# Kernel tuning notes

Measured on AMD Instinct MI355X. Metric: run time of the kernel, lower is better.

The kernel has to match this reference:

```python
import jax, jax.numpy as jnp
import numpy as np

N = 50000      # nodes
E = 800000     # edges
F_IN = 512     # num_features
H = 128        # hidden


def setup_inputs() -> dict:
    key = jax.random.key(0)
    ks = jax.random.split(key, 10)
    edge_index = jax.random.randint(ks[0], (2, E), 0, N, dtype=jnp.int64 if jax.config.jax_enable_x64 else jnp.int32)
    x = jax.random.normal(ks[1], (N, F_IN), jnp.float32)
    weights = jax.random.uniform(ks[2], (E,), jnp.float32)
    def w(i, shape, fan):
        return jax.random.normal(ks[i], shape, jnp.float32) / np.sqrt(fan).astype(np.float32)
    return {
        "edge_index": edge_index,
        "x": x,
        "weights": weights,
        "W_lin1": w(3, (F_IN, H), F_IN), "b_lin1": jnp.zeros((H,), jnp.float32),
        "W_conv1": w(4, (H, 2 * H), H), "b_conv1": jnp.zeros((2 * H,), jnp.float32),
        "W_mu": w(5, (2 * H, H), 2 * H), "b_mu": jnp.zeros((H,), jnp.float32),
        "W_lin": w(6, (2 * H, 1), 2 * H), "b_lin": jnp.zeros((1,), jnp.float32),
    }


def gcn_conv(x, W, b, src, dst, ew, n):
    """PyG GCNConv with edge weights: add self-loops (weight 1), symmetric norm, scatter-add."""
    loop = jnp.arange(n, dtype=src.dtype)
    s2 = jnp.concatenate([src, loop])
    d2 = jnp.concatenate([dst, loop])
    w2 = jnp.concatenate([ew, jnp.ones((n,), x.dtype)])
    deg = jax.ops.segment_sum(w2, d2, num_segments=n)          # weighted in-degree incl. self-loop
    dinv = jnp.where(deg > 0, deg, 1.0) ** -0.5
    dinv = jnp.where(deg > 0, dinv, 0.0)
    norm = dinv[s2] * w2 * dinv[d2]                            # [E+N]
    h = x @ W                                                   # [N, out]
    out = jax.ops.segment_sum(h[s2] * norm[:, None], d2, num_segments=n)
    return out + b


def reference(edge_index, x, weights, W_lin1, b_lin1, W_conv1, b_conv1, W_mu, b_mu, W_lin, b_lin):
    n = x.shape[0]
    src, dst = edge_index[0], edge_index[1]
    # eval mode: dropout is identity, VGAE.encode returns mu
    h = x @ W_lin1 + b_lin1                                     # lin1
    h = jax.nn.relu(gcn_conv(h, W_conv1, b_conv1, src, dst, weights, n))
    z = gcn_conv(h, W_mu, b_mu, src, dst, weights, n)           # mu == embeddings
    emb_edges = jnp.concatenate([z[src], z[dst]], axis=1)       # [E, 2H]
    out = jax.nn.sigmoid(emb_edges @ W_lin + b_lin)
    return out.squeeze(-1)                                      # [E]
```

## Files before the change

### kernel.cpp

```cpp
#include <hip/hip_runtime.h>
#include <hip/hip_bf16.h>
#include <math.h>


#define NSL 256
#define RSH 8
#define RNG 256

typedef __attribute__((ext_vector_type(8))) short bf16x8;
typedef __attribute__((ext_vector_type(4))) float f32x4;

static __device__ __forceinline__ ushort f2b(float f) {
    __hip_bfloat16 h = __float2bfloat16(f);
    return *(ushort*)&h;
}
static __device__ __forceinline__ float b2f(ushort u) {
    unsigned int v = ((unsigned int)u) << 16;
    return *(float*)&v;
}
static __device__ __forceinline__ bf16x8 cvt8(float4 a, float4 b) {
    bf16x8 r;
    r[0] = (short)f2b(a.x); r[1] = (short)f2b(a.y); r[2] = (short)f2b(a.z); r[3] = (short)f2b(a.w);
    r[4] = (short)f2b(b.x); r[5] = (short)f2b(b.y); r[6] = (short)f2b(b.z); r[7] = (short)f2b(b.w);
    return r;
}


__global__ __launch_bounds__(256) void bucket_count(const int* __restrict__ dst,
                                                    int* __restrict__ cntA, int E, int NR) {
    __shared__ int lc[256];
    const int b = blockIdx.x, t = threadIdx.x;
    lc[t] = 0;
    __syncthreads();
    const int beg = (int)((long long)b * E / NSL);
    const int end = (int)((long long)(b + 1) * E / NSL);
    for (int e = beg + t; e < end; e += 256) atomicAdd(&lc[dst[e] >> RSH], 1);
    __syncthreads();
    if (t < NR) cntA[b * NR + t] = lc[t];
}

__global__ __launch_bounds__(256) void range_scan(int* __restrict__ cntA,
                                                  int* __restrict__ rtot, int NR) {
    __shared__ int s_[256];
    const int r = blockIdx.x, t = threadIdx.x;
    int v = cntA[t * NR + r];
    s_[t] = v;
    __syncthreads();
    for (int off = 1; off < 256; off <<= 1) {
        int add = (t >= off) ? s_[t - off] : 0;
        __syncthreads();
        s_[t] += add;
        __syncthreads();
    }
    cntA[t * NR + r] = s_[t] - v;
    if (t == 255) rtot[r] = s_[t];
}

__global__ __launch_bounds__(256) void base_scan(const int* __restrict__ rtot,
                                                 int* __restrict__ baseOut, int NR) {
    __shared__ int s_[256];
    const int t = threadIdx.x;
    int v = (t < NR) ? rtot[t] : 0;
    s_[t] = v;
    __syncthreads();
    for (int off = 1; off < 256; off <<= 1) {
        int add = (t >= off) ? s_[t - off] : 0;
        __syncthreads();
        s_[t] += add;
        __syncthreads();
    }
    if (t < NR) baseOut[t] = s_[t] - v;
    if (t == NR - 1) baseOut[NR] = s_[t];
}

__global__ __launch_bounds__(256) void bucket_scatter(const int* __restrict__ src,
                                                      const int* __restrict__ dst,
                                                      const float* __restrict__ w,
                                                      const int* __restrict__ cntA,
                                                      const int* __restrict__ baseOut,
                                                      unsigned int* __restrict__ packB,
                                                      float* __restrict__ wB, int E, int NR) {
    __shared__ int cur[256];
    const int b = blockIdx.x, t = threadIdx.x;
    if (t < NR) cur[t] = cntA[b * NR + t] + baseOut[t];
    __syncthreads();
    const int beg = (int)((long long)b * E / NSL);
    const int end = (int)((long long)(b + 1) * E / NSL);
    for (int e = beg + t; e < end; e += 256) {
        int d = dst[e];
        int r = d >> RSH;
        int pos = atomicAdd(&cur[r], 1);
        packB[pos] = ((unsigned int)(d & (RNG - 1)) << 24) | (unsigned int)src[e];
        wB[pos] = w[e];
    }
}

__global__ __launch_bounds__(256) void range_deg(const unsigned int* __restrict__ packB,
                                                 const float* __restrict__ wB,
                                                 const int* __restrict__ baseOut,
                                                 float* __restrict__ dinv,
                                                 int* __restrict__ offs,
                                                 int N, int E) {
    __shared__ float lw[256];
    __shared__ int lc[256];
    __shared__ int sc[256];
    const int r = blockIdx.x, t = threadIdx.x;
    lw[t] = 0.f; lc[t] = 0;
    __syncthreads();
    const int beg = baseOut[r], end = baseOut[r + 1];
    for (int e = beg + t; e < end; e += 256) {
        unsigned int pk = packB[e];
        int dl = pk >> 24;
        atomicAdd(&lc[dl], 1);
        atomicAdd(&lw[dl], wB[e]);
    }
    __syncthreads();
    int v = lc[t];
    sc[t] = v;
    __syncthreads();
    for (int off = 1; off < 256; off <<= 1) {
        int add = (t >= off) ? sc[t - off] : 0;
        __syncthreads();
        sc[t] += add;
        __syncthreads();
    }
    int node = (r << RSH) + t;
    if (node < N) {
        dinv[node] = 1.0f / sqrtf(1.0f + lw[t]);
        offs[node] = beg + sc[t] - v;
    }
    if (r == 0 && t == 0) offs[N] = E;
}

__global__ __launch_bounds__(256) void csr_build(const unsigned int* __restrict__ packB,
                                                 const float* __restrict__ wB,
                                                 const int* __restrict__ baseOut,
                                                 const float* __restrict__ dinv,
                                                 const int* __restrict__ offs,
                                                 int* __restrict__ es,
                                                 float* __restrict__ en, int N) {
    __shared__ int cur[256];
    __shared__ float ldv[256];
    const int r = blockIdx.x, t = threadIdx.x;
    const int node = (r << RSH) + t;
    cur[t] = (node < N) ? offs[node] : 0;
    ldv[t] = (node < N) ? dinv[node] : 0.f;
    __syncthreads();
    const int beg = baseOut[r], end = baseOut[r + 1];
    for (int e = beg + t; e < end; e += 256) {
        unsigned int pk = packB[e];
        int dl = pk >> 24;
        int s = pk & 0xFFFFFF;
        float nrm = dinv[s] * wB[e] * ldv[dl];
        int pos = atomicAdd(&cur[dl], 1);
        es[pos] = s;
        en[pos] = nrm;
    }
}


__global__ __launch_bounds__(256) void tconv_kernel(const float* __restrict__ B,
                                                    ushort* __restrict__ BT, int K, int Nn) {
    int i = blockIdx.x * 256 + threadIdx.x;
    if (i < K * Nn) {
        int k = i / Nn, n = i % Nn;
        BT[(size_t)n * K + k] = f2b(B[i]);
    }
}

__global__ __launch_bounds__(256) void fold_kernel(const float* __restrict__ Wm,
                                                   const float* __restrict__ Wl,
                                                   const float* __restrict__ bm,
                                                   float* __restrict__ wmp,
                                                   float* __restrict__ wmq,
                                                   float* __restrict__ bpq) {
    int j = threadIdx.x;
    float sp = 0.f, sq = 0.f;
    for (int k = 0; k < 128; ++k) {
        float v = Wm[(size_t)j * 128 + k];
        sp += v * Wl[k];
        sq += v * Wl[128 + k];
    }
    wmp[j] = sp; wmq[j] = sq;
    if (j == 0) { float s = 0.f; for (int k = 0; k < 128; ++k) s += bm[k] * Wl[k];       bpq[0] = s; }
    if (j == 1) { float s = 0.f; for (int k = 0; k < 128; ++k) s += bm[k] * Wl[128 + k]; bpq[1] = s; }
}

__global__ __launch_bounds__(64) void gemm1_stream(const float* __restrict__ A,
                                                   const ushort* __restrict__ BT,
                                                   const float* __restrict__ bias,
                                                   ushort* __restrict__ C, int M) {
    const int lane = threadIdx.x;
    const int r0 = blockIdx.x * 16;
    const int lrow = lane & 15;
    const int lk   = (lane >> 4) * 8;

    f32x4 acc[8] = {};

    const float*  a  = A  + (size_t)min(r0 + lrow, M - 1) * 512 + lk;
    const ushort* bp = BT + (size_t)lrow * 512 + lk;

#pragma unroll 4
    for (int ks = 0; ks < 16; ++ks) {
        const int k0 = ks * 32;
        float4 aa = *(const float4*)(a + k0);
        float4 ab = *(const float4*)(a + k0 + 4);
        bf16x8 af = cvt8(aa, ab);
#pragma unroll
        for (int ni = 0; ni < 8; ++ni) {
            bf16x8 bfr = *(const bf16x8*)(bp + (size_t)ni * 16 * 512 + k0);
            acc[ni] = __builtin_amdgcn_mfma_f32_16x16x32_bf16(af, bfr, acc[ni], 0, 0, 0);
        }
    }

#pragma unroll
    for (int ni = 0; ni < 8; ++ni) {
        int col = ni * 16 + lrow;
        float bv = bias[col];
#pragma unroll
        for (int r = 0; r < 4; ++r) {
            int row = r0 + (lane >> 4) * 4 + r;
            if (row < M) C[(size_t)row * 128 + col] = f2b(acc[ni][r] + bv);
        }
    }
}

__global__ __launch_bounds__(256) void aggregate_bf16(const ushort* __restrict__ h,
                                                      const int* __restrict__ offs,
                                                      const int* __restrict__ es,
                                                      const float* __restrict__ en,
                                                      const float* __restrict__ dinv,
                                                      ushort* __restrict__ out, int n) {
    int wave = (int)((blockIdx.x * (size_t)blockDim.x + threadIdx.x) >> 6);
    int lane = threadIdx.x & 63;
    if (wave >= n) return;
    float di = dinv[wave];
    float sw = di * di;
    unsigned int hv = *(const unsigned int*)(h + (size_t)wave * 128 + lane * 2);
    float ax = sw * b2f((ushort)(hv & 0xffff));
    float ay = sw * b2f((ushort)(hv >> 16));
    int beg = offs[wave], end = offs[wave + 1];
    for (int e = beg; e < end; e += 8) {
        int sx[8]; float wx[8];
#pragma unroll
        for (int j = 0; j < 8; ++j) {
            bool v = (e + j) < end;
            sx[j] = v ? es[e + j] : wave;
            wx[j] = v ? en[e + j] : 0.f;
        }
        unsigned int vv[8];
#pragma unroll
        for (int j = 0; j < 8; ++j)
            vv[j] = *(const unsigned int*)(h + (size_t)sx[j] * 128 + lane * 2);
#pragma unroll
        for (int j = 0; j < 8; ++j) {
            ax += wx[j] * b2f((ushort)(vv[j] & 0xffff));
            ay += wx[j] * b2f((ushort)(vv[j] >> 16));
        }
    }
    unsigned int o = (unsigned int)f2b(ax) | ((unsigned int)f2b(ay) << 16);
    *(unsigned int*)(out + (size_t)wave * 128 + lane * 2) = o;
}

__global__ __launch_bounds__(64) void gemm2_stream(const ushort* __restrict__ A,
                                                   const ushort* __restrict__ BT,
                                                   const float* __restrict__ bc,
                                                   const float* __restrict__ wmp,
                                                   const float* __restrict__ wmq,
                                                   float* __restrict__ pe,
                                                   float* __restrict__ qe, int M) {
    const int lane = threadIdx.x;
    const int r0 = blockIdx.x * 16;
    const int lrow = lane & 15;
    const int lk   = (lane >> 4) * 8;

    f32x4 acc[16] = {};

    const ushort* a  = A  + (size_t)min(r0 + lrow, M - 1) * 128 + lk;
    const ushort* bp = BT + (size_t)lrow * 128 + lk;

#pragma unroll
    for (int ks = 0; ks < 4; ++ks) {
        const int k0 = ks * 32;
        bf16x8 af = *(const bf16x8*)(a + k0);
#pragma unroll
        for (int ni = 0; ni < 16; ++ni) {
            bf16x8 bfr = *(const bf16x8*)(bp + (size_t)ni * 16 * 128 + k0);
            acc[ni] = __builtin_amdgcn_mfma_f32_16x16x32_bf16(af, bfr, acc[ni], 0, 0, 0);
        }
    }

    float bcv[16], wpv[16], wqv[16];
#pragma unroll
    for (int ni = 0; ni < 16; ++ni) {
        int col = ni * 16 + lrow;
        bcv[ni] = bc[col];
        wpv[ni] = wmp[col];
        wqv[ni] = wmq[col];
    }
#pragma unroll
    for (int r = 0; r < 4; ++r) {
        float sp = 0.f, sq = 0.f;
#pragma unroll
        for (int ni = 0; ni < 16; ++ni) {
            float h = fmaxf(acc[ni][r] + bcv[ni], 0.f);
            sp += h * wpv[ni];
            sq += h * wqv[ni];
        }
#pragma unroll
        for (int off = 1; off < 16; off <<= 1) {
            sp += __shfl_xor(sp, off);
            sq += __shfl_xor(sq, off);
        }
        if (lrow == 0) {
            int row = r0 + (lane >> 4) * 4 + r;
            if (row < M) { pe[row] = sp; qe[row] = sq; }
        }
    }
}

__global__ __launch_bounds__(256) void agg_scalar(const float* __restrict__ pe,
                                                  const float* __restrict__ qe,
                                                  const int* __restrict__ offs,
                                                  const int* __restrict__ es,
                                                  const float* __restrict__ en,
                                                  const float* __restrict__ dinv,
                                                  const float* __restrict__ bpq,
                                                  float* __restrict__ p,
                                                  float* __restrict__ q, int n) {
    int i = blockIdx.x * 256 + threadIdx.x;
    if (i >= n) return;
    float di = dinv[i];
    float sw = di * di;
    float ap = sw * pe[i], aq = sw * qe[i];
    int beg = offs[i], end = offs[i + 1];
    for (int k = beg; k < end; k += 4) {
        int sx[4]; float wx[4];
#pragma unroll
        for (int j = 0; j < 4; ++j) {
            bool v = (k + j) < end;
            sx[j] = v ? es[k + j] : i;
            wx[j] = v ? en[k + j] : 0.f;
        }
        float pv[4], qv[4];
#pragma unroll
        for (int j = 0; j < 4; ++j) { pv[j] = pe[sx[j]]; qv[j] = qe[sx[j]]; }
#pragma unroll
        for (int j = 0; j < 4; ++j) { ap += wx[j] * pv[j]; aq += wx[j] * qv[j]; }
    }
    p[i] = ap + bpq[0];
    q[i] = aq + bpq[1];
}

__global__ __launch_bounds__(256) void edge_out_kernel(const int* __restrict__ src,
                                                       const int* __restrict__ dst,
                                                       const float* __restrict__ p,
                                                       const float* __restrict__ q,
                                                       const float* __restrict__ bl,
                                                       float* __restrict__ out, int e) {
    int i = blockIdx.x * 256 + threadIdx.x;
    if (i < e) {
        float t = p[src[i]] + q[dst[i]] + bl[0];
        out[i] = 1.0f / (1.0f + expf(-t));
    }
}


extern "C" void kernel_launch(void* const* d_in, const int* in_sizes, int n_in,
                              void* d_out, int out_size, void* d_ws, size_t ws_size,
                              hipStream_t stream) {
    const int*   edge_index = (const int*)d_in[0];
    const float* x   = (const float*)d_in[1];
    const float* w   = (const float*)d_in[2];
    const float* W1  = (const float*)d_in[3];
    const float* b1  = (const float*)d_in[4];
    const float* Wc  = (const float*)d_in[5];
    const float* bc  = (const float*)d_in[6];
    const float* Wm  = (const float*)d_in[7];
    const float* bm  = (const float*)d_in[8];
    const float* Wl  = (const float*)d_in[9];
    const float* bl  = (const float*)d_in[10];
    float* out = (float*)d_out;

    const int E  = in_sizes[2];
    const int H  = in_sizes[4];
    const int F  = in_sizes[3] / H;
    const int N  = in_sizes[1] / F;
    const int H2 = 2 * H;
    const int NR = (N + RNG - 1) / RNG;

    const int* src = edge_index;
    const int* dst = edge_index + E;

    char* ws = (char*)d_ws;
    size_t off = 0;
    auto alloc = [&](size_t bytes) -> void* {
        off = (off + 255) & ~(size_t)255;
        void* r = ws + off;
        off += bytes;
        return r;
    };
    int*          cntA    = (int*)         alloc((size_t)NSL * NR * 4);
    int*          rtot    = (int*)         alloc((size_t)NR * 4);
    int*          baseOut = (int*)         alloc((size_t)(NR + 1) * 4);
    unsigned int* packB   = (unsigned int*)alloc((size_t)E * 4);
    float*        wB      = (float*)       alloc((size_t)E * 4);
    float*        dinv    = (float*)       alloc((size_t)N * 4);
    int*          offs    = (int*)         alloc((size_t)(N + 1) * 4);
    int*          es      = (int*)         alloc((size_t)E * 4);
    float*        en      = (float*)       alloc((size_t)E * 4);
    ushort*       h0_bf   = (ushort*)      alloc((size_t)N * H * 2);
    ushort*       agg1_bf = (ushort*)      alloc((size_t)N * H * 2);
    ushort*       W1T     = (ushort*)      alloc((size_t)H * F * 2);
    ushort*       WcT     = (ushort*)      alloc((size_t)H2 * H * 2);
    float*        wmp     = (float*)       alloc(H2 * 4);
    float*        wmq     = (float*)       alloc(H2 * 4);
    float*        bpq     = (float*)       alloc(2 * 4);
    float*        pe      = (float*)       alloc((size_t)N * 4);
    float*        qe      = (float*)       alloc((size_t)N * 4);
    float*        p       = (float*)       alloc((size_t)N * 4);
    float*        q       = (float*)       alloc((size_t)N * 4);
    (void)ws_size; (void)n_in; (void)out_size;

    int nbN  = (N + 255) / 256;
    int nbE  = (E + 255) / 256;
    int nbW  = (int)(((size_t)N * 64 + 255) / 256);
    int nb16 = (N + 15) / 16;

    bucket_count<<<NSL, 256, 0, stream>>>(dst, cntA, E, NR);
    range_scan<<<NR, 256, 0, stream>>>(cntA, rtot, NR);
    base_scan<<<1, 256, 0, stream>>>(rtot, baseOut, NR);
    bucket_scatter<<<NSL, 256, 0, stream>>>(src, dst, w, cntA, baseOut, packB, wB, E, NR);
    range_deg<<<NR, 256, 0, stream>>>(packB, wB, baseOut, dinv, offs, N, E);
    csr_build<<<NR, 256, 0, stream>>>(packB, wB, baseOut, dinv, offs, es, en, N);

    tconv_kernel<<<(F * H + 255) / 256, 256, 0, stream>>>(W1, W1T, F, H);
    tconv_kernel<<<(H * H2 + 255) / 256, 256, 0, stream>>>(Wc, WcT, H, H2);
    fold_kernel<<<1, 256, 0, stream>>>(Wm, Wl, bm, wmp, wmq, bpq);

    gemm1_stream<<<nb16, 64, 0, stream>>>(x, W1T, b1, h0_bf, N);
    aggregate_bf16<<<nbW, 256, 0, stream>>>(h0_bf, offs, es, en, dinv, agg1_bf, N);
    gemm2_stream<<<nb16, 64, 0, stream>>>(agg1_bf, WcT, bc, wmp, wmq, pe, qe, N);
    agg_scalar<<<nbN, 256, 0, stream>>>(pe, qe, offs, es, en, dinv, bpq, p, q, N);
    edge_out_kernel<<<nbE, 256, 0, stream>>>(src, dst, p, q, bl, out, E);
}
```

Measured before the change: 213.7 us.

## Tile gemm1 through LDS with direct global-to-LDS loads and swizzling

Replaces the single-wave, 16-row streaming GEMM for x@W_lin1 with a 256-thread block that computes a 64x128 output tile. The block stages A (fp32) and W1T (bf16) through shared memory using global_load_lds with XOR swizzling to avoid bank conflicts. Each W1T tile is now loaded once per 64 rows instead of once per 16 rows, which cuts redundant weight traffic and global-to-register latency. The cost is two barriers per K step with no double buffering, fewer blocks, and extra LDS use that may limit occupancy.

```diff
diff --git a/kernel.cpp b/kernel.cpp
--- a/kernel.cpp
+++ b/kernel.cpp
@@ -9,6 +9,13 @@
 
 typedef __attribute__((ext_vector_type(8))) short bf16x8;
 typedef __attribute__((ext_vector_type(4))) float f32x4;
+
+typedef const __attribute__((address_space(1))) unsigned int* gas_t;
+typedef __attribute__((address_space(3))) unsigned int* las_t;
+
+static __device__ __forceinline__ void gload_lds16(const void* g, void* l) {
+    __builtin_amdgcn_global_load_lds((gas_t)g, (las_t)l, 16, 0, 0);
+}
 
 static __device__ __forceinline__ ushort f2b(float f) {
     __hip_bfloat16 h = __float2bfloat16(f);
@@ -186,42 +193,87 @@
     if (j == 1) { float s = 0.f; for (int k = 0; k < 128; ++k) s += bm[k] * Wl[128 + k]; bpq[1] = s; }
 }
 
-__global__ __launch_bounds__(64) void gemm1_stream(const float* __restrict__ A,
-                                                   const ushort* __restrict__ BT,
-                                                   const float* __restrict__ bias,
-                                                   ushort* __restrict__ C, int M) {
-    const int lane = threadIdx.x;
-    const int r0 = blockIdx.x * 16;
-    const int lrow = lane & 15;
-    const int lk   = (lane >> 4) * 8;
-
-    f32x4 acc[8] = {};
-
-    const float*  a  = A  + (size_t)min(r0 + lrow, M - 1) * 512 + lk;
-    const ushort* bp = BT + (size_t)lrow * 512 + lk;
-
-#pragma unroll 4
-    for (int ks = 0; ks < 16; ++ks) {
-        const int k0 = ks * 32;
-        float4 aa = *(const float4*)(a + k0);
-        float4 ab = *(const float4*)(a + k0 + 4);
-        bf16x8 af = cvt8(aa, ab);
-#pragma unroll
-        for (int ni = 0; ni < 8; ++ni) {
-            bf16x8 bfr = *(const bf16x8*)(bp + (size_t)ni * 16 * 512 + k0);
-            acc[ni] = __builtin_amdgcn_mfma_f32_16x16x32_bf16(af, bfr, acc[ni], 0, 0, 0);
-        }
-    }
-
-#pragma unroll
-    for (int ni = 0; ni < 8; ++ni) {
-        int col = ni * 16 + lrow;
+__global__ __launch_bounds__(256) void gemm1_mfma(const float* __restrict__ A,
+                                                  const ushort* __restrict__ BT,
+                                                  const float* __restrict__ bias,
+                                                  ushort* __restrict__ C, int M) {
+    __shared__ float  As[64 * 64];
+    __shared__ ushort Bs[128 * 64];
+    char* AsB = (char*)As;
+    char* BsB = (char*)Bs;
+    const int t = threadIdx.x;
+    const int bm = blockIdx.x * 64;
+    const int lane = t & 63;
+    const int wid = t >> 6;
+    const int wm = (wid >> 1) * 32, wn = (wid & 1) * 64;
+
+    f32x4 acc[2][4] = {};
+
+    const int a_row_l = (lane >> 4);
+    const int a_ib    = (lane & 15) * 16;
+    const int b_row_l = (lane >> 3);
+    const int b_ib    = (lane & 7) * 16;
+
+#pragma unroll 1
+    for (int tt = 0; tt < 8; ++tt) {
+        const int k0 = tt * 64;
+#pragma unroll
+        for (int j = 0; j < 4; ++j) {
+            int c = wid * 4 + j;
+            int row = c * 4 + a_row_l;
+            int sw = a_ib ^ ((row & 7) << 5);
+            int grow = min(bm + row, M - 1);
+            const char* src = (const char*)A + ((size_t)grow * 512 + k0) * 4 + sw;
+            gload_lds16(src, AsB + c * 1024);
+        }
+#pragma unroll
+        for (int j = 0; j < 4; ++j) {
+            int c = wid * 4 + j;
+            int row = c * 8 + b_row_l;
+            int sw = b_ib ^ ((row & 7) << 4);
+            const char* src = (const char*)BT + (size_t)row * 1024 + k0 * 2 + sw;
+            gload_lds16(src, BsB + c * 1024);
+        }
+        __syncthreads();
+#pragma unroll
+        for (int ks = 0; ks < 2; ++ks) {
+            bf16x8 af[2], bfr[4];
+#pragma unroll
+            for (int mi = 0; mi < 2; ++mi) {
+                int r = wm + mi * 16 + (lane & 15);
+                int byte = r * 256 + ks * 128 + (lane >> 4) * 32;
+                byte ^= (r & 7) << 5;
+                float4 f0 = *(const float4*)(AsB + byte);
+                float4 f1 = *(const float4*)(AsB + byte + 16);
+                af[mi] = cvt8(f0, f1);
+            }
+#pragma unroll
+            for (int ni = 0; ni < 4; ++ni) {
+                int r = wn + ni * 16 + (lane & 15);
+                int byte = r * 128 + ks * 64 + (lane >> 4) * 16;
+                byte ^= (r & 7) << 4;
+                bfr[ni] = *(const bf16x8*)(BsB + byte);
+            }
+#pragma unroll
+            for (int mi = 0; mi < 2; ++mi)
+#pragma unroll
+                for (int ni = 0; ni < 4; ++ni)
+                    acc[mi][ni] = __builtin_amdgcn_mfma_f32_16x16x32_bf16(af[mi], bfr[ni], acc[mi][ni], 0, 0, 0);
+        }
+        __syncthreads();
+    }
+
+#pragma unroll
+    for (int ni = 0; ni < 4; ++ni) {
+        int col = wn + ni * 16 + (lane & 15);
         float bv = bias[col];
 #pragma unroll
-        for (int r = 0; r < 4; ++r) {
-            int row = r0 + (lane >> 4) * 4 + r;
-            if (row < M) C[(size_t)row * 128 + col] = f2b(acc[ni][r] + bv);
-        }
+        for (int mi = 0; mi < 2; ++mi)
+#pragma unroll
+            for (int r = 0; r < 4; ++r) {
+                int row = bm + wm + mi * 16 + (lane >> 4) * 4 + r;
+                if (row < M) C[(size_t)row * 128 + col] = f2b(acc[mi][ni][r] + bv);
+            }
     }
 }
 
@@ -425,6 +477,7 @@
     int nbN  = (N + 255) / 256;
     int nbE  = (E + 255) / 256;
     int nbW  = (int)(((size_t)N * 64 + 255) / 256);
+    int nb64 = (N + 63) / 64;
     int nb16 = (N + 15) / 16;
 
     bucket_count<<<NSL, 256, 0, stream>>>(dst, cntA, E, NR);
@@ -438,7 +491,7 @@
     tconv_kernel<<<(H * H2 + 255) / 256, 256, 0, stream>>>(Wc, WcT, H, H2);
     fold_kernel<<<1, 256, 0, stream>>>(Wm, Wl, bm, wmp, wmq, bpq);
 
-    gemm1_stream<<<nb16, 64, 0, stream>>>(x, W1T, b1, h0_bf, N);
+    gemm1_mfma<<<nb64, 256, 0, stream>>>(x, W1T, b1, h0_bf, N);
     aggregate_bf16<<<nbW, 256, 0, stream>>>(h0_bf, offs, es, en, dinv, agg1_bf, N);
     gemm2_stream<<<nb16, 64, 0, stream>>>(agg1_bf, WcT, bc, wmp, wmq, pe, qe, N);
     agg_scalar<<<nbN, 256, 0, stream>>>(pe, qe, offs, es, en, dinv, bpq, p, q, N);
```

New measurement: 184.2 us. 1.16x faster.
